# Kernel tuning notes

Measured on AMD Instinct MI355X. Metric: run time of the kernel, lower is better.

The kernel has to match this reference:

```python
import jax, jax.numpy as jnp
import numpy as np

B, N, L, D, DI = 128, 64, 33, 512, 768  # batch, num_images, cooccurrence_num+1, CLIP dim, inst dim


def setup_inputs() -> dict:
    key = jax.random.key(0)
    ks = jax.random.split(key, 8)
    return {
        "image_features": jax.random.normal(ks[0], (B, N, D), jnp.float32),
        "image_mask": jax.random.randint(ks[1], (B, N), 0, 2).astype(jnp.int32),
        "landmark_feature": jax.random.normal(ks[2], (B, L, D), jnp.float32),
        "inst": jax.random.normal(ks[3], (B, DI), jnp.float32),
        # scoring_module = Linear(512+768 -> 512) -> ReLU -> LayerNorm(512) -> Dropout(eval: identity)
        "W_score": jax.random.normal(ks[4], (DI + D, D), jnp.float32) * 0.02,
        "b_score": jnp.zeros((D,), jnp.float32),
        "ln_gamma": jnp.ones((D,), jnp.float32),
        "ln_beta": jnp.zeros((D,), jnp.float32),
    }


def _l2norm(x):
    return x / jnp.linalg.norm(x, axis=-1, keepdims=True)


def reference(image_features, image_mask, landmark_feature, inst,
              W_score, b_score, ln_gamma, ln_beta):
    LN_EPS = 1e-12
    mask = image_mask == 1  # [B, N]

    img = _l2norm(image_features)          # [B, N, D]
    lmk = _l2norm(landmark_feature)        # [B, L, D]
    img = jnp.where(mask[:, :, None], img, 0.0)
    img_mean = img.mean(axis=1)            # [B, D]

    # scoring_module on cat([inst, img_mean]) -> ReLU -> LayerNorm (Dropout is identity in eval)
    h = jnp.concatenate([inst, img_mean], axis=-1) @ W_score + b_score  # [B, D]
    h = jax.nn.relu(h)
    mu = h.mean(axis=-1, keepdims=True)
    var = h.var(axis=-1, keepdims=True)    # biased, as in torch LayerNorm
    h = (h - mu) / jnp.sqrt(var + LN_EPS) * ln_gamma + ln_beta
    inst_feat = _l2norm(h)                 # [B, D]

    cooccurrence_weight = 100.0 * jnp.einsum('bd,bld->bl', inst_feat, lmk)  # [B, L]
    candidate_prob = 100.0 * jnp.einsum('bnd,bld->bnl', img, lmk)           # [B, N, L]
    candidate_prob = jnp.where(mask[:, :, None], candidate_prob, -jnp.inf)
    p = jax.nn.softmax(candidate_prob, axis=1)                              # softmax over images

    corrected_landmark_feature = jnp.einsum('bnl,bl,bld->bnd', p, cooccurrence_weight, lmk)  # [B, N, D]
    corrected_candidate_prob = jnp.einsum('bnl,bl->bn', p, cooccurrence_weight)              # [B, N]
    corrected_candidate_prob = jnp.where(mask, corrected_candidate_prob, -jnp.inf)
    return corrected_landmark_feature, corrected_candidate_prob
```

## Files before the change

kernel.cpp:

```cpp
#include <hip/hip_runtime.h>
#include <math.h>

#define BB 128
#define NN 64
#define LL 33
#define DD 512
#define DIN 768

#define NEG_BIG (-3.0e38f)

typedef __attribute__((ext_vector_type(8))) short bf16x8;
typedef __attribute__((ext_vector_type(4))) float f32x4;

#define WS_ASW   0
#define WS_BSW   (WS_ASW + BB*3*16*64*4)
#define WS_LMK16 (WS_BSW + BB*4*16*64*4)
#define WS_MEANP (WS_LMK16 + BB*LL*DD/2)
#define WS_PART  (WS_MEANP + BB*16*DD)
#define WS_INSTF (WS_PART + BB*8*DD)
#define WS_S     (WS_INSTF + BB*DD)

__device__ __forceinline__ float wave_sum(float v) {
#pragma unroll
  for (int m = 32; m; m >>= 1) v += __shfl_xor(v, m);
  return v;
}
__device__ __forceinline__ float wave_max(float v) {
#pragma unroll
  for (int m = 32; m; m >>= 1) v = fmaxf(v, __shfl_xor(v, m));
  return v;
}
__device__ __forceinline__ unsigned f2bf(float f) {
  unsigned u = __float_as_uint(f);
  return (u + 0x7FFFu + ((u >> 16) & 1u)) >> 16;
}
__device__ __forceinline__ unsigned pk2(float a, float b) {
  return f2bf(a) | (f2bf(b) << 16);
}
__device__ __forceinline__ float bflo(unsigned u) { return __uint_as_float(u << 16); }
__device__ __forceinline__ float bfhi(unsigned u) { return __uint_as_float(u & 0xFFFF0000u); }

__global__ __launch_bounds__(256) void k_prep_v14(
    const float* __restrict__ img_in, const int* __restrict__ mask,
    const float* __restrict__ lmk_in, unsigned int* __restrict__ AswW,
    unsigned int* __restrict__ BswW, unsigned short* __restrict__ lmk16,
    float* __restrict__ meanp) {
  uint4* Asw = (uint4*)AswW;
  uint4* Bsw = (uint4*)BswW;
  int o = blockIdx.x;
  int blk = (o & 7) * 64 + (o >> 3);
  int b = blk >> 2, q = blk & 3;
  int t = threadIdx.x;
  int w = t >> 6, lane = t & 63;

  int nbase = q * 16 + w * 4;
  const float4* ib = (const float4*)(img_in + ((size_t)b * NN + nbase) * DD);
  float4 r[4][2];
#pragma unroll
  for (int i = 0; i < 4; i++) {
    r[i][0] = ib[i * 128 + lane * 2];
    r[i][1] = ib[i * 128 + lane * 2 + 1];
  }
  const int* mb = mask + b * NN + nbase;
  float macc[8];
#pragma unroll
  for (int j = 0; j < 8; j++) macc[j] = 0.f;
#pragma unroll
  for (int i = 0; i < 4; i++) {
    float4 v0 = r[i][0], v1 = r[i][1];
    float ss = v0.x * v0.x + v0.y * v0.y + v0.z * v0.z + v0.w * v0.w +
               v1.x * v1.x + v1.y * v1.y + v1.z * v1.z + v1.w * v1.w;
    ss = wave_sum(ss);
    float keep = (mb[i] == 1) ? 1.f : 0.f;
    float s = keep / sqrtf(ss);
    v0.x *= s; v0.y *= s; v0.z *= s; v0.w *= s;
    v1.x *= s; v1.y *= s; v1.z *= s; v1.w *= s;
    macc[0] += v0.x; macc[1] += v0.y; macc[2] += v0.z; macc[3] += v0.w;
    macc[4] += v1.x; macc[5] += v1.y; macc[6] += v1.z; macc[7] += v1.w;
    int rg = nbase + i;
    uint4 p = make_uint4(pk2(v0.x, v0.y), pk2(v0.z, v0.w), pk2(v1.x, v1.y),
                         pk2(v1.z, v1.w));
    Bsw[(((size_t)b * 4 + (rg >> 4)) * 16 + (lane >> 2)) * 64 + (rg & 15) +
        16 * (lane & 3)] = p;
  }
  {
    float* mp = meanp + ((size_t)b * 16 + q * 4 + w) * DD + lane * 8;
    float4 m0 = {macc[0], macc[1], macc[2], macc[3]};
    float4 m1 = {macc[4], macc[5], macc[6], macc[7]};
    *(float4*)mp = m0;
    *(float4*)(mp + 4) = m1;
  }

  int lr = q * 8 + w * 2;
  bool xtra = (q == 0) && (w == 3);
  if (xtra) {
#pragma unroll
    for (int kk = 0; kk < 16; kk++)
      if (lane & 15)
        Asw[(((size_t)b * 3 + 2) * 16 + kk) * 64 + lane] = make_uint4(0, 0, 0, 0);
  }
#pragma unroll
  for (int k = 0; k < 3; k++) {
    int row = (k < 2) ? (lr + k) : 32;
    if (k == 2 && !xtra) break;
    const float4* lb = (const float4*)(lmk_in + ((size_t)b * LL + row) * DD);
    float4 v0 = lb[lane * 2], v1 = lb[lane * 2 + 1];
    float ss = v0.x * v0.x + v0.y * v0.y + v0.z * v0.z + v0.w * v0.w +
               v1.x * v1.x + v1.y * v1.y + v1.z * v1.z + v1.w * v1.w;
    ss = wave_sum(ss);
    float s = 1.f / sqrtf(ss);
    v0.x *= s; v0.y *= s; v0.z *= s; v0.w *= s;
    v1.x *= s; v1.y *= s; v1.z *= s; v1.w *= s;
    uint4 p = make_uint4(pk2(v0.x, v0.y), pk2(v0.z, v0.w), pk2(v1.x, v1.y),
                         pk2(v1.z, v1.w));
    ((uint4*)lmk16)[((size_t)b * LL + row) * 64 + lane] = p;
    Asw[(((size_t)b * 3 + (row >> 4)) * 16 + (lane >> 2)) * 64 + (row & 15) +
        16 * (lane & 3)] = p;
  }
}

__global__ __launch_bounds__(256) void k_S_mfma_v14(
    const unsigned int* __restrict__ AswW, const unsigned int* __restrict__ BswW,
    float* __restrict__ S) {
  const bf16x8* Asw = (const bf16x8*)AswW;
  const bf16x8* Bsw = (const bf16x8*)BswW;
  int o = blockIdx.x;
  int blk = (o & 7) * 48 + (o >> 3);
  int b = blk / 3, mt = blk - b * 3;
  int t = threadIdx.x;
  int nt = t >> 6, lane = t & 63;

  const bf16x8* ap = Asw + ((size_t)(b * 3 + mt) * 16) * 64 + lane;
  const bf16x8* bp = Bsw + ((size_t)(b * 4 + nt) * 16) * 64 + lane;
  f32x4 acc = {0.f, 0.f, 0.f, 0.f};
#pragma unroll
  for (int kk = 0; kk < 16; kk++)
    acc = __builtin_amdgcn_mfma_f32_16x16x32_bf16(ap[kk * 64], bp[kk * 64], acc,
                                                  0, 0, 0);
  int n = nt * 16 + (lane & 15);
  int rowbase = mt * 16 + ((lane >> 4) << 2);
#pragma unroll
  for (int reg = 0; reg < 4; reg++) {
    int l = rowbase + reg;
    if (l < LL) S[((size_t)b * LL + l) * NN + n] = 100.f * acc[reg];
  }
}

#define KCH 160
__global__ void k_gemm_part_v14(const float* __restrict__ inst,
                                const float* __restrict__ meanp,
                                const float* __restrict__ W,
                                float* __restrict__ part) {
  int o = blockIdx.x;
  int blk = (o & 7) * 32 + (o >> 3);
  __shared__ float xs[KCH][4];
  int bg = blk >> 3;
  int c = blk & 7;
  int b0 = bg * 4;
  int t = threadIdx.x;
  int k0 = c * KCH;
  for (int i = t; i < KCH * 4; i += 256) {
    int kk = i >> 2;
    int j = i & 3;
    int kg = k0 + kk;
    float val;
    if (kg < DIN) {
      val = inst[(size_t)(b0 + j) * DIN + kg];
    } else {
      const float* mp = meanp + (size_t)(b0 + j) * 16 * DD + (kg - DIN);
      float s = 0.f;
#pragma unroll
      for (int p = 0; p < 16; p++) s += mp[p * DD];
      val = s * (1.f / 64.f);
    }
    xs[kk][j] = val;
  }
  __syncthreads();
  const float2* Wp = (const float2*)(W + (size_t)k0 * DD);
  float2 a0 = {0.f, 0.f}, a1 = {0.f, 0.f}, a2 = {0.f, 0.f}, a3 = {0.f, 0.f};
#pragma unroll 4
  for (int kk = 0; kk < KCH; kk++) {
    float2 w = Wp[kk * 256 + t];
    float4 xv = *(const float4*)&xs[kk][0];
    a0.x += xv.x * w.x; a0.y += xv.x * w.y;
    a1.x += xv.y * w.x; a1.y += xv.y * w.y;
    a2.x += xv.z * w.x; a2.y += xv.z * w.y;
    a3.x += xv.w * w.x; a3.y += xv.w * w.y;
  }
  float2* pp = (float2*)part;
  pp[(((size_t)(b0 + 0) * 8 + c) * DD >> 1) + t] = a0;
  pp[(((size_t)(b0 + 1) * 8 + c) * DD >> 1) + t] = a1;
  pp[(((size_t)(b0 + 2) * 8 + c) * DD >> 1) + t] = a2;
  pp[(((size_t)(b0 + 3) * 8 + c) * DD >> 1) + t] = a3;
}

__device__ __forceinline__ float blk_sum512(float v, float* red, int t) {
  v = wave_sum(v);
  __syncthreads();
  if ((t & 63) == 0) red[t >> 6] = v;
  __syncthreads();
  return red[0] + red[1] + red[2] + red[3] + red[4] + red[5] + red[6] + red[7];
}

__global__ void k_score_fin_v14(const float* __restrict__ part,
                                const float* __restrict__ bias,
                                const float* __restrict__ gamma,
                                const float* __restrict__ beta,
                                float* __restrict__ instf) {
  __shared__ float red[8];
  int o = blockIdx.x;
  int b = (o & 7) * 16 + (o >> 3);
  int d = threadIdx.x;
  const float* pb = part + (size_t)b * 8 * DD + d;
  float s = 0.f;
#pragma unroll
  for (int c = 0; c < 8; c++) s += pb[c * DD];
  float rv = fmaxf(s + bias[d], 0.f);
  float s1 = blk_sum512(rv, red, d);
  float s2 = blk_sum512(rv * rv, red, d);
  float mu = s1 * (1.f / DD);
  float var = s2 * (1.f / DD) - mu * mu;
  float inv = 1.f / sqrtf(var + 1e-12f);
  float y = (rv - mu) * inv * gamma[d] + beta[d];
  float n2 = blk_sum512(y * y, red, d);
  instf[(size_t)b * DD + d] = y * (1.f / sqrtf(n2));
}

__global__ void k_colsm_v14(const float* __restrict__ instf,
                            const unsigned short* __restrict__ lmk16,
                            const int* __restrict__ mask,
                            float* __restrict__ S) {
  int o = blockIdx.x;
  int blk = (o & 7) * 528 + (o >> 3);
  int b = blk / LL;
  int l = blk - b * LL;
  int lane = threadIdx.x;
  size_t rowbase = ((size_t)b * LL + l) * NN;
  float s = S[rowbase + lane];
  bool keep = (mask[b * NN + lane] == 1);
  const float* fi = instf + (size_t)b * DD;
  float4 ai = ((const float4*)fi)[lane * 2];
  float4 bi = ((const float4*)fi)[lane * 2 + 1];
  uint4 u = ((const uint4*)(lmk16 + ((size_t)b * LL + l) * DD))[lane];
  float dp = ai.x * bflo(u.x) + ai.y * bfhi(u.x) + ai.z * bflo(u.y) +
             ai.w * bfhi(u.y) + bi.x * bflo(u.z) + bi.y * bfhi(u.z) +
             bi.z * bflo(u.w) + bi.w * bfhi(u.w);
  dp = wave_sum(dp);
  float cw = 100.f * dp;
  float v = keep ? s : NEG_BIG;
  float mx = wave_max(v);
  float e = keep ? __expf(s - mx) : 0.f;
  float Z = wave_sum(e);
  float sc = (Z > 0.f) ? (cw / Z) : 0.f;
  S[rowbase + lane] = e * sc;
}

__global__ void k_out_v14(const float* __restrict__ S,
                          const unsigned short* __restrict__ lmk16,
                          const int* __restrict__ mask,
                          float* __restrict__ out1,
                          float* __restrict__ out2) {
  __shared__ __align__(16) float qs[LL][8];
  int o = blockIdx.x;
  int blk = (o & 7) * 128 + (o >> 3);
  int b = blk >> 3;
  int nt = blk & 7;
  int t = threadIdx.x;
  for (int i = t; i < 8 * LL; i += 256) {
    int l = i >> 3;
    int n_loc = i & 7;
    qs[l][n_loc] = S[((size_t)b * LL + l) * NN + nt * 8 + n_loc];
  }
  __syncthreads();
  if (t < 8) {
    float ssum = 0.f;
#pragma unroll
    for (int l = 0; l < LL; l++) ssum += qs[l][t];
    int n = nt * 8 + t;
    out2[b * NN + n] = (mask[b * NN + n] == 1) ? ssum : NEG_BIG;
  }
  int d0 = t * 2;
  float accx[8], accy[8];
#pragma unroll
  for (int n = 0; n < 8; n++) { accx[n] = 0.f; accy[n] = 0.f; }
  const unsigned short* lmkb = lmk16 + (size_t)b * LL * DD;
#pragma unroll 4
  for (int l = 0; l < LL; l++) {
    unsigned u = *(const unsigned*)(lmkb + (size_t)l * DD + d0);
    float lvx = bflo(u), lvy = bfhi(u);
    float4 q0 = *(const float4*)&qs[l][0];
    float4 q1 = *(const float4*)&qs[l][4];
    accx[0] += q0.x * lvx; accy[0] += q0.x * lvy;
    accx[1] += q0.y * lvx; accy[1] += q0.y * lvy;
    accx[2] += q0.z * lvx; accy[2] += q0.z * lvy;
    accx[3] += q0.w * lvx; accy[3] += q0.w * lvy;
    accx[4] += q1.x * lvx; accy[4] += q1.x * lvy;
    accx[5] += q1.y * lvx; accy[5] += q1.y * lvy;
    accx[6] += q1.z * lvx; accy[6] += q1.z * lvy;
    accx[7] += q1.w * lvx; accy[7] += q1.w * lvy;
  }
#pragma unroll
  for (int n = 0; n < 8; n++) {
    float2 oo = {accx[n], accy[n]};
    *(float2*)&out1[(((size_t)b * NN) + nt * 8 + n) * DD + d0] = oo;
  }
}

extern "C" void kernel_launch(void* const* d_in, const int* in_sizes, int n_in,
                              void* d_out, int out_size, void* d_ws, size_t ws_size,
                              hipStream_t stream) {
  const float* image_features = (const float*)d_in[0];
  const int* image_mask = (const int*)d_in[1];
  const float* landmark = (const float*)d_in[2];
  const float* inst = (const float*)d_in[3];
  const float* W = (const float*)d_in[4];
  const float* bias = (const float*)d_in[5];
  const float* gamma = (const float*)d_in[6];
  const float* beta = (const float*)d_in[7];

  float* ws = (float*)d_ws;
  unsigned int* Asw = (unsigned int*)(ws + WS_ASW);
  unsigned int* Bsw = (unsigned int*)(ws + WS_BSW);
  unsigned short* lmk16 = (unsigned short*)(ws + WS_LMK16);
  float* ws_meanp = ws + WS_MEANP;
  float* ws_part = ws + WS_PART;
  float* ws_instf = ws + WS_INSTF;
  float* ws_S = ws + WS_S;

  float* out1 = (float*)d_out;
  float* out2 = (float*)d_out + (size_t)BB * NN * DD;

  k_prep_v14<<<BB * 4, 256, 0, stream>>>(image_features, image_mask, landmark,
                                         Asw, Bsw, lmk16, ws_meanp);
  k_gemm_part_v14<<<(BB / 4) * 8, 256, 0, stream>>>(inst, ws_meanp, W, ws_part);
  k_score_fin_v14<<<BB, 512, 0, stream>>>(ws_part, bias, gamma, beta, ws_instf);
  k_S_mfma_v14<<<BB * 3, 256, 0, stream>>>(Asw, Bsw, ws_S);
  k_colsm_v14<<<BB * LL, 64, 0, stream>>>(ws_instf, lmk16, image_mask, ws_S);
  k_out_v14<<<BB * 8, 256, 0, stream>>>(ws_S, lmk16, image_mask, out1, out2);
}
```

Measured before the change: 51.70 us.

## Fuse score finalize, MFMA similarity, and column softmax into one kernel

Merges three kernels (LayerNorm/L2 finalize of the scoring output, the bf16 MFMA image–landmark similarity, and the per-landmark softmax/co-occurrence weighting) into a single kernel per (batch, 16-row tile). The S tile stays in shared memory instead of going through global memory, and the normalized instruction feature lives in shared memory. This removes two launches and a global round trip of S. In exchange, each of the three tiles per batch redundantly recomputes the LayerNorm finalize, and the grid is smaller.

```diff
diff --git a/kernel.cpp b/kernel.cpp
--- a/kernel.cpp
+++ b/kernel.cpp
@@ -40,7 +40,7 @@
 __device__ __forceinline__ float bflo(unsigned u) { return __uint_as_float(u << 16); }
 __device__ __forceinline__ float bfhi(unsigned u) { return __uint_as_float(u & 0xFFFF0000u); }
 
-__global__ __launch_bounds__(256) void k_prep_v14(
+__global__ __launch_bounds__(256) void k_prep_v15(
     const float* __restrict__ img_in, const int* __restrict__ mask,
     const float* __restrict__ lmk_in, unsigned int* __restrict__ AswW,
     unsigned int* __restrict__ BswW, unsigned short* __restrict__ lmk16,
@@ -119,35 +119,8 @@
   }
 }
 
-__global__ __launch_bounds__(256) void k_S_mfma_v14(
-    const unsigned int* __restrict__ AswW, const unsigned int* __restrict__ BswW,
-    float* __restrict__ S) {
-  const bf16x8* Asw = (const bf16x8*)AswW;
-  const bf16x8* Bsw = (const bf16x8*)BswW;
-  int o = blockIdx.x;
-  int blk = (o & 7) * 48 + (o >> 3);
-  int b = blk / 3, mt = blk - b * 3;
-  int t = threadIdx.x;
-  int nt = t >> 6, lane = t & 63;
-
-  const bf16x8* ap = Asw + ((size_t)(b * 3 + mt) * 16) * 64 + lane;
-  const bf16x8* bp = Bsw + ((size_t)(b * 4 + nt) * 16) * 64 + lane;
-  f32x4 acc = {0.f, 0.f, 0.f, 0.f};
-#pragma unroll
-  for (int kk = 0; kk < 16; kk++)
-    acc = __builtin_amdgcn_mfma_f32_16x16x32_bf16(ap[kk * 64], bp[kk * 64], acc,
-                                                  0, 0, 0);
-  int n = nt * 16 + (lane & 15);
-  int rowbase = mt * 16 + ((lane >> 4) << 2);
-#pragma unroll
-  for (int reg = 0; reg < 4; reg++) {
-    int l = rowbase + reg;
-    if (l < LL) S[((size_t)b * LL + l) * NN + n] = 100.f * acc[reg];
-  }
-}
-
 #define KCH 160
-__global__ void k_gemm_part_v14(const float* __restrict__ inst,
+__global__ void k_gemm_part_v15(const float* __restrict__ inst,
                                 const float* __restrict__ meanp,
                                 const float* __restrict__ W,
                                 float* __restrict__ part) {
@@ -194,68 +167,94 @@
   pp[(((size_t)(b0 + 3) * 8 + c) * DD >> 1) + t] = a3;
 }
 
-__device__ __forceinline__ float blk_sum512(float v, float* red, int t) {
+__device__ __forceinline__ float blk_sum2(float v, float* red4, int t) {
   v = wave_sum(v);
   __syncthreads();
-  if ((t & 63) == 0) red[t >> 6] = v;
-  __syncthreads();
-  return red[0] + red[1] + red[2] + red[3] + red[4] + red[5] + red[6] + red[7];
-}
-
-__global__ void k_score_fin_v14(const float* __restrict__ part,
-                                const float* __restrict__ bias,
-                                const float* __restrict__ gamma,
-                                const float* __restrict__ beta,
-                                float* __restrict__ instf) {
-  __shared__ float red[8];
+  if ((t & 63) == 0) red4[t >> 6] = v;
+  __syncthreads();
+  return red4[0] + red4[1] + red4[2] + red4[3];
+}
+
+__global__ __launch_bounds__(256) void k_ssm_v15(
+    const unsigned int* __restrict__ AswW, const unsigned int* __restrict__ BswW,
+    const float* __restrict__ part, const float* __restrict__ bias,
+    const float* __restrict__ gamma, const float* __restrict__ beta,
+    const unsigned short* __restrict__ lmk16, const int* __restrict__ mask,
+    float* __restrict__ q) {
+  __shared__ float st[16][68];
+  __shared__ float fi[DD];
+  __shared__ float red4[4];
+  const bf16x8* Asw = (const bf16x8*)AswW;
+  const bf16x8* Bsw = (const bf16x8*)BswW;
   int o = blockIdx.x;
-  int b = (o & 7) * 16 + (o >> 3);
-  int d = threadIdx.x;
-  const float* pb = part + (size_t)b * 8 * DD + d;
-  float s = 0.f;
-#pragma unroll
-  for (int c = 0; c < 8; c++) s += pb[c * DD];
-  float rv = fmaxf(s + bias[d], 0.f);
-  float s1 = blk_sum512(rv, red, d);
-  float s2 = blk_sum512(rv * rv, red, d);
-  float mu = s1 * (1.f / DD);
-  float var = s2 * (1.f / DD) - mu * mu;
-  float inv = 1.f / sqrtf(var + 1e-12f);
-  float y = (rv - mu) * inv * gamma[d] + beta[d];
-  float n2 = blk_sum512(y * y, red, d);
-  instf[(size_t)b * DD + d] = y * (1.f / sqrtf(n2));
-}
-
-__global__ void k_colsm_v14(const float* __restrict__ instf,
-                            const unsigned short* __restrict__ lmk16,
-                            const int* __restrict__ mask,
-                            float* __restrict__ S) {
-  int o = blockIdx.x;
-  int blk = (o & 7) * 528 + (o >> 3);
-  int b = blk / LL;
-  int l = blk - b * LL;
-  int lane = threadIdx.x;
-  size_t rowbase = ((size_t)b * LL + l) * NN;
-  float s = S[rowbase + lane];
+  int blk = (o & 7) * 48 + (o >> 3);
+  int b = blk / 3, mt = blk - b * 3;
+  int t = threadIdx.x;
+  int nt = t >> 6, lane = t & 63;
+
+  {
+    const float* pb = part + (size_t)b * 8 * DD;
+    float sa = 0.f, sb = 0.f;
+#pragma unroll
+    for (int c = 0; c < 8; c++) {
+      sa += pb[c * DD + t];
+      sb += pb[c * DD + t + 256];
+    }
+    float rva = fmaxf(sa + bias[t], 0.f);
+    float rvb = fmaxf(sb + bias[t + 256], 0.f);
+    float s1 = blk_sum2(rva + rvb, red4, t);
+    float s2 = blk_sum2(rva * rva + rvb * rvb, red4, t);
+    float mu = s1 * (1.f / DD);
+    float var = s2 * (1.f / DD) - mu * mu;
+    float inv = 1.f / sqrtf(var + 1e-12f);
+    float ya = (rva - mu) * inv * gamma[t] + beta[t];
+    float yb = (rvb - mu) * inv * gamma[t + 256] + beta[t + 256];
+    float n2 = blk_sum2(ya * ya + yb * yb, red4, t);
+    float rn = 1.f / sqrtf(n2);
+    fi[t] = ya * rn;
+    fi[t + 256] = yb * rn;
+  }
+
+  {
+    const bf16x8* ap = Asw + ((size_t)(b * 3 + mt) * 16) * 64 + lane;
+    const bf16x8* bp = Bsw + ((size_t)(b * 4 + nt) * 16) * 64 + lane;
+    f32x4 acc = {0.f, 0.f, 0.f, 0.f};
+#pragma unroll
+    for (int kk = 0; kk < 16; kk++)
+      acc = __builtin_amdgcn_mfma_f32_16x16x32_bf16(ap[kk * 64], bp[kk * 64],
+                                                    acc, 0, 0, 0);
+    int col = nt * 16 + (lane & 15);
+    int rbase = (lane >> 4) << 2;
+#pragma unroll
+    for (int reg = 0; reg < 4; reg++) st[rbase + reg][col] = 100.f * acc[reg];
+  }
+  __syncthreads();
+
   bool keep = (mask[b * NN + lane] == 1);
-  const float* fi = instf + (size_t)b * DD;
-  float4 ai = ((const float4*)fi)[lane * 2];
-  float4 bi = ((const float4*)fi)[lane * 2 + 1];
-  uint4 u = ((const uint4*)(lmk16 + ((size_t)b * LL + l) * DD))[lane];
-  float dp = ai.x * bflo(u.x) + ai.y * bfhi(u.x) + ai.z * bflo(u.y) +
-             ai.w * bfhi(u.y) + bi.x * bflo(u.z) + bi.y * bfhi(u.z) +
-             bi.z * bflo(u.w) + bi.w * bfhi(u.w);
-  dp = wave_sum(dp);
-  float cw = 100.f * dp;
-  float v = keep ? s : NEG_BIG;
-  float mx = wave_max(v);
-  float e = keep ? __expf(s - mx) : 0.f;
-  float Z = wave_sum(e);
-  float sc = (Z > 0.f) ? (cw / Z) : 0.f;
-  S[rowbase + lane] = e * sc;
-}
-
-__global__ void k_out_v14(const float* __restrict__ S,
+  const float4* fi4 = (const float4*)fi;
+  float4 f0 = fi4[lane * 2], f1 = fi4[lane * 2 + 1];
+#pragma unroll
+  for (int j = 0; j < 4; j++) {
+    int lrow = nt * 4 + j;
+    int l = mt * 16 + lrow;
+    if (l >= LL) break;
+    float s = st[lrow][lane];
+    uint4 u = ((const uint4*)(lmk16 + ((size_t)b * LL + l) * DD))[lane];
+    float dp = f0.x * bflo(u.x) + f0.y * bfhi(u.x) + f0.z * bflo(u.y) +
+               f0.w * bfhi(u.y) + f1.x * bflo(u.z) + f1.y * bfhi(u.z) +
+               f1.z * bflo(u.w) + f1.w * bfhi(u.w);
+    dp = wave_sum(dp);
+    float cw = 100.f * dp;
+    float v = keep ? s : NEG_BIG;
+    float mx = wave_max(v);
+    float e = keep ? __expf(s - mx) : 0.f;
+    float Z = wave_sum(e);
+    float sc = (Z > 0.f) ? (cw / Z) : 0.f;
+    q[((size_t)b * LL + l) * NN + lane] = e * sc;
+  }
+}
+
+__global__ void k_out_v15(const float* __restrict__ S,
                           const unsigned short* __restrict__ lmk16,
                           const int* __restrict__ mask,
                           float* __restrict__ out1,
@@ -324,17 +323,16 @@
   unsigned short* lmk16 = (unsigned short*)(ws + WS_LMK16);
   float* ws_meanp = ws + WS_MEANP;
   float* ws_part = ws + WS_PART;
-  float* ws_instf = ws + WS_INSTF;
   float* ws_S = ws + WS_S;
 
   float* out1 = (float*)d_out;
   float* out2 = (float*)d_out + (size_t)BB * NN * DD;
 
-  k_prep_v14<<<BB * 4, 256, 0, stream>>>(image_features, image_mask, landmark,
+  k_prep_v15<<<BB * 4, 256, 0, stream>>>(image_features, image_mask, landmark,
                                          Asw, Bsw, lmk16, ws_meanp);
-  k_gemm_part_v14<<<(BB / 4) * 8, 256, 0, stream>>>(inst, ws_meanp, W, ws_part);
-  k_score_fin_v14<<<BB, 512, 0, stream>>>(ws_part, bias, gamma, beta, ws_instf);
-  k_S_mfma_v14<<<BB * 3, 256, 0, stream>>>(Asw, Bsw, ws_S);
-  k_colsm_v14<<<BB * LL, 64, 0, stream>>>(ws_instf, lmk16, image_mask, ws_S);
-  k_out_v14<<<BB * 8, 256, 0, stream>>>(ws_S, lmk16, image_mask, out1, out2);
-}
+  k_gemm_part_v15<<<(BB / 4) * 8, 256, 0, stream>>>(inst, ws_meanp, W, ws_part);
+  k_ssm_v15<<<BB * 3, 256, 0, stream>>>((const unsigned int*)Asw,
+                                        (const unsigned int*)Bsw, ws_part, bias,
+                                        gamma, beta, lmk16, image_mask, ws_S);
+  k_out_v15<<<BB * 8, 256, 0, stream>>>(ws_S, lmk16, image_mask, out1, out2);
+}
```

Result: faster. 48.96 us (-5.3%).
